# Kernel optimization log

Hardware: AMD Instinct MI355X
Metric: run time of the kernel (lower is better)

The kernel has to match this reference:

```python
import jax, jax.numpy as jnp
import numpy as np

# Closed-form 2-qubit circuit: |00> -> RY(a) on q0, RY(b) on q1 -> CNOT(0,1) -> RY(theta) on q0,
# then measure <Z0>,<Z1>, output (Z+1)/2. torchquantum wire0 = most significant bit.

PIXELS = 3072
N_PAIRS = 460
N_CLASSES = 10
BATCH = 1024


def setup_inputs() -> dict:
    key = jax.random.key(0)
    k1, k2, k3 = jax.random.split(key, 3)
    x = jax.random.normal(k1, (BATCH, 3, 32, 32), dtype=jnp.float32)
    theta = jax.random.normal(k2, (N_CLASSES,), dtype=jnp.float32)  # per-class RY angle
    pair_idx = jax.random.randint(k3, (BATCH, N_PAIRS, 2), 0, PIXELS)
    return {"x": x, "theta": theta, "pair_idx": pair_idx}


def reference(x, theta, pair_idx):
    B = x.shape[0]
    flat = x.reshape(B, -1)  # [B, 3072]
    # gather paired pixel values: [B, P, 2]
    vals = jnp.take_along_axis(flat, pair_idx.reshape(B, -1), axis=1).reshape(B, N_PAIRS, 2)
    a = vals[..., 0]  # angle for qubit 0
    b = vals[..., 1]  # angle for qubit 1
    ca, sa = jnp.cos(a / 2), jnp.sin(a / 2)
    cb, sb = jnp.cos(b / 2), jnp.sin(b / 2)
    # state after RY(a)xRY(b) then CNOT(ctrl=0, tgt=1): swap |10><->|11>
    psi00 = ca * cb
    psi01 = ca * sb
    psi10 = sa * sb  # was psi11
    psi11 = sa * cb  # was psi10
    # RY(theta) on qubit 0, per class: broadcast [B,P,1] x [C]
    ct = jnp.cos(theta / 2)[None, None, :]
    st = jnp.sin(theta / 2)[None, None, :]
    p00 = ct * psi00[..., None] - st * psi10[..., None]
    p10 = st * psi00[..., None] + ct * psi10[..., None]
    p01 = ct * psi01[..., None] - st * psi11[..., None]
    p11 = st * psi01[..., None] + ct * psi11[..., None]
    q00, q01, q10, q11 = p00 * p00, p01 * p01, p10 * p10, p11 * p11
    z0 = q00 + q01 - q10 - q11  # <Z> on wire 0
    z1 = q00 - q01 + q10 - q11  # <Z> on wire 1
    qout = (jnp.stack([z0, z1], axis=2) + 1.0) / 2.0  # [B, P, 2, C]
    return qout.reshape(B, N_PAIRS * 2, N_CLASSES)
```

## Files before the change

### kernel.cpp

```cpp
#include <hip/hip_runtime.h>

#define NPAIRS 460
#define NCLASS 10
#define PIX    3072
#define BATCH  1024
#define TPB    512
#define NF4    (NPAIRS * 5)

__global__ __launch_bounds__(TPB) void
qmem_kernel(const float* __restrict__ x,
            const float* __restrict__ theta,
            const int2*  __restrict__ pidx,
            float4* __restrict__ out)
{
    __shared__ float s_x[PIX];
    __shared__ int2  s_pi[NPAIRS];
    __shared__ float s_ct[NCLASS], s_st[NCLASS];

    const int b = blockIdx.x;
    const int t = threadIdx.x;

    const float2* xrow = (const float2*)(x + (size_t)b * PIX);
#pragma unroll
    for (int i = 0; i < 3; ++i) {
        int j = t + i * TPB;
        float2 v = xrow[j];
        s_x[2 * j]     = v.x;
        s_x[2 * j + 1] = v.y;
    }
    const int2* prow = pidx + (size_t)b * NPAIRS;
    if (t < NPAIRS) s_pi[t] = prow[t];
    if (t < NCLASS) {
        float s, c;
        __sincosf(theta[t], &s, &c);
        s_ct[t] = c;
        s_st[t] = s;
    }
    __syncthreads();

    float4* og = out + (size_t)b * NF4;
    for (int j = t; j < NF4; j += TPB) {
        int p = j / 5;
        int k = (j - p * 5) * 4;
        int2 pi = s_pi[p];
        float sa, ca, sb, cb;
        __sincosf(s_x[pi.x], &sa, &ca);
        __sincosf(s_x[pi.y], &sb, &cb);
        float sasb = sa * sb;
        float o1   = fmaf(0.5f, ca * cb, 0.5f);

        float4 v;
        float* vp = (float*)&v;
#pragma unroll
        for (int e = 0; e < 4; ++e) {
            int c = k + e;
            if (c < NCLASS) {
                vp[e] = fmaf(0.5f, s_ct[c] * ca - s_st[c] * sasb, 0.5f);
            } else {
                vp[e] = o1;
            }
        }
        og[j] = v;
    }
}

extern "C" void kernel_launch(void* const* d_in, const int* in_sizes, int n_in,
                              void* d_out, int out_size, void* d_ws, size_t ws_size,
                              hipStream_t stream) {
    const float* x     = (const float*)d_in[0];
    const float* theta = (const float*)d_in[1];
    const int2*  pidx  = (const int2*)d_in[2];
    float4* out = (float4*)d_out;

    qmem_kernel<<<BATCH, TPB, 0, stream>>>(x, theta, pidx, out);
}
```

Before: 14.98 us.

## Process two rows per block with async LDS double-buffered staging

Each block now handles two batch rows and stages image rows into LDS with direct global-to-LDS loads. The next row is prefetched into a second buffer while the current one is computed. Pair indices are read straight from global memory instead of being staged in shared memory. This is meant to hide row-load latency and cut launch/staging overhead, at the cost of halving the number of blocks and depending on correct wait semantics for the async loads.

```diff
diff --git a/kernel.cpp b/kernel.cpp
--- a/kernel.cpp
+++ b/kernel.cpp
@@ -5,7 +5,22 @@
 #define PIX    3072
 #define BATCH  1024
 #define TPB    512
+#define RPB    2
 #define NF4    (NPAIRS * 5)
+
+__device__ __forceinline__ void stage_row(const float* __restrict__ xrow,
+                                          float* __restrict__ lds_buf,
+                                          int wave, int lane)
+{
+    for (int c = wave; c < 12; c += 8) {
+        const float* gp = xrow + c * 256 + lane * 4;
+        float*       lp = lds_buf + c * 256;
+        __builtin_amdgcn_global_load_lds(
+            (const __attribute__((address_space(1))) unsigned int*)((const void*)gp),
+            (__attribute__((address_space(3))) unsigned int*)((void*)lp),
+            16, 0, 0);
+    }
+}
 
 __global__ __launch_bounds__(TPB) void
 qmem_kernel(const float* __restrict__ x,
@@ -13,54 +28,57 @@
             const int2*  __restrict__ pidx,
             float4* __restrict__ out)
 {
-    __shared__ float s_x[PIX];
-    __shared__ int2  s_pi[NPAIRS];
+    __shared__ float s_x[2][PIX];
     __shared__ float s_ct[NCLASS], s_st[NCLASS];
 
-    const int b = blockIdx.x;
-    const int t = threadIdx.x;
+    const int t    = threadIdx.x;
+    const int wave = t >> 6;
+    const int lane = t & 63;
+    const int row0 = blockIdx.x * RPB;
 
-    const float2* xrow = (const float2*)(x + (size_t)b * PIX);
-#pragma unroll
-    for (int i = 0; i < 3; ++i) {
-        int j = t + i * TPB;
-        float2 v = xrow[j];
-        s_x[2 * j]     = v.x;
-        s_x[2 * j + 1] = v.y;
-    }
-    const int2* prow = pidx + (size_t)b * NPAIRS;
-    if (t < NPAIRS) s_pi[t] = prow[t];
     if (t < NCLASS) {
         float s, c;
         __sincosf(theta[t], &s, &c);
         s_ct[t] = c;
         s_st[t] = s;
     }
+
+    stage_row(x + (size_t)row0 * PIX, &s_x[0][0], wave, lane);
     __syncthreads();
 
-    float4* og = out + (size_t)b * NF4;
-    for (int j = t; j < NF4; j += TPB) {
-        int p = j / 5;
-        int k = (j - p * 5) * 4;
-        int2 pi = s_pi[p];
-        float sa, ca, sb, cb;
-        __sincosf(s_x[pi.x], &sa, &ca);
-        __sincosf(s_x[pi.y], &sb, &cb);
-        float sasb = sa * sb;
-        float o1   = fmaf(0.5f, ca * cb, 0.5f);
+    for (int r = 0; r < RPB; ++r) {
+        const int row = row0 + r;
+        const int cur = r & 1;
 
-        float4 v;
-        float* vp = (float*)&v;
+        if (r + 1 < RPB)
+            stage_row(x + (size_t)(row + 1) * PIX, &s_x[cur ^ 1][0], wave, lane);
+
+        const float* sx   = &s_x[cur][0];
+        const int2*  prow = pidx + (size_t)row * NPAIRS;
+        float4*      og   = out + (size_t)row * NF4;
+
+        for (int j = t; j < NF4; j += TPB) {
+            int p = j / 5;
+            int k = (j - p * 5) * 4;
+            int2 pi = prow[p];
+            float sa, ca, sb, cb;
+            __sincosf(sx[pi.x], &sa, &ca);
+            __sincosf(sx[pi.y], &sb, &cb);
+            float sasb = sa * sb;
+            float o1   = fmaf(0.5f, ca * cb, 0.5f);
+
+            float4 v;
+            float* vp = (float*)&v;
 #pragma unroll
-        for (int e = 0; e < 4; ++e) {
-            int c = k + e;
-            if (c < NCLASS) {
-                vp[e] = fmaf(0.5f, s_ct[c] * ca - s_st[c] * sasb, 0.5f);
-            } else {
-                vp[e] = o1;
+            for (int e = 0; e < 4; ++e) {
+                int c = k + e;
+                vp[e] = (c < NCLASS)
+                      ? fmaf(0.5f, s_ct[c] * ca - s_st[c] * sasb, 0.5f)
+                      : o1;
             }
+            og[j] = v;
         }
-        og[j] = v;
+        __syncthreads();
     }
 }
 
@@ -72,5 +90,5 @@
     const int2*  pidx  = (const int2*)d_in[2];
     float4* out = (float4*)d_out;
 
-    qmem_kernel<<<BATCH, TPB, 0, stream>>>(x, theta, pidx, out);
+    qmem_kernel<<<BATCH / RPB, TPB, 0, stream>>>(x, theta, pidx, out);
 }
```

Result: slower. 17.06 us (+13.9%).
